# Kernel optimization log

Hardware: AMD Instinct MI355X
Metric: run time of the kernel (lower is better)

The kernel has to match this reference:

```python
import jax, jax.numpy as jnp
import numpy as np

B, NW, WL, CH, D, H, L, FF = 8, 1024, 8, 4, 512, 8, 4, 2048
K = 512  # num_masked = int(0.5 * NW)
SCALE = (D // H) ** -0.5


def _ln(x, g, b):
    m = jnp.mean(x, -1, keepdims=True)
    v = jnp.var(x, -1, keepdims=True)
    return (x - m) * jax.lax.rsqrt(v + 1e-5) * g + b


def setup_inputs():
    key = jax.random.key(0)
    ks = jax.random.split(key, 16)
    n = lambda i, shape, s=0.02: jax.random.normal(ks[i], shape, jnp.float32) * s
    return {
        "seq": jax.random.normal(ks[0], (B, NW * WL, CH), jnp.float32),
        "mask_idx": jax.lax.top_k(jax.random.uniform(ks[1], (B, NW)), K)[1].astype(jnp.int32),
        "pos_embedding": n(2, (1, NW + 1, D)),
        "mask_token": jax.random.normal(ks[3], (D,), jnp.float32),
        "pln1_g": jnp.ones((WL * CH,)), "pln1_b": jnp.zeros((WL * CH,)),
        "W_emb": n(4, (WL * CH, D)), "b_emb": jnp.zeros((D,)),
        "pln2_g": jnp.ones((D,)), "pln2_b": jnp.zeros((D,)),
        "aln_g": jnp.ones((L, D)), "aln_b": jnp.zeros((L, D)),
        "Wqkv": n(5, (L, D, 3 * D)),
        "Wo": n(6, (L, D, D)),
        "fln_g": jnp.ones((L, D)), "fln_b": jnp.zeros((L, D)),
        "Wff1": n(7, (L, D, FF)), "bff1": jnp.zeros((L, FF)),
        "Wff2": n(8, (L, FF, D)), "bff2": jnp.zeros((L, D)),
        "oln_g": jnp.ones((D,)), "oln_b": jnp.zeros((D,)),
        "W_words": n(9, (D, WL * CH)), "b_words": jnp.zeros((WL * CH,)),
    }


def reference(seq, mask_idx, pos_embedding, mask_token, pln1_g, pln1_b, W_emb, b_emb,
              pln2_g, pln2_b, aln_g, aln_b, Wqkv, Wo, fln_g, fln_b, Wff1, bff1,
              Wff2, bff2, oln_g, oln_b, W_words, b_words):
    b = seq.shape[0]
    words = seq.reshape(b, NW, WL * CH)                       # to_patch: 'b (n w) c -> b n (w c)'
    pos = pos_embedding[:, 1:NW + 1]                          # [1, NW, D]
    tokens = _ln(_ln(words, pln1_g, pln1_b) @ W_emb + b_emb, pln2_g, pln2_b) + pos
    mask_tokens = mask_token + pos                            # [1, NW, D] broadcast over batch
    bool_mask = jnp.zeros((b, NW), bool).at[jnp.arange(b)[:, None], mask_idx].set(True)
    tokens = jnp.where(bool_mask[..., None], mask_tokens, tokens)

    def block(x, p):
        h = _ln(x, p["ag"], p["ab"])
        q, k, v = [t.reshape(b, NW, H, D // H) for t in jnp.split(h @ p["Wqkv"], 3, axis=-1)]
        attn = jax.nn.softmax(jnp.einsum("bihd,bjhd->bhij", q, k) * SCALE, axis=-1)
        o = jnp.einsum("bhij,bjhd->bihd", attn, v).reshape(b, NW, D)
        x = x + o @ p["Wo"]
        h = _ln(x, p["fg"], p["fb"])
        x = x + jax.nn.gelu(h @ p["W1"] + p["b1"]) @ p["W2"] + p["b2"]
        return x, None

    layer_params = {"ag": aln_g, "ab": aln_b, "Wqkv": Wqkv, "Wo": Wo,
                    "fg": fln_g, "fb": fln_b, "W1": Wff1, "b1": bff1,
                    "W2": Wff2, "b2": bff2}
    encoded, _ = jax.lax.scan(block, tokens, layer_params)
    encoded = _ln(encoded, oln_g, oln_b)

    idx = mask_idx[..., None]
    enc_m = jnp.take_along_axis(encoded, idx, axis=1)         # [b, K, D] gather of masked positions
    pred = jax.nn.softmax((enc_m @ W_words + b_words).reshape(b, K, WL, CH), axis=-1)
    labels = jnp.take_along_axis(words, idx, axis=1).reshape(b, K, WL, CH)
    return pred, labels
```

## Files before the change

kernel.cpp:

```cpp
#include <hip/hip_runtime.h>
#include <hip/hip_bf16.h>
#include <stdint.h>


#define NTOK 8192
#define DMODEL 512
#define NHEAD 8
#define DHEAD 64
#define NWIN 1024
#define NBATCH 8
#define KMASK 512
#define FFDIM 2048
#define NLAYER 4

typedef __bf16 bf16x8 __attribute__((ext_vector_type(8)));
typedef float f32x4 __attribute__((ext_vector_type(4)));

#define MFMA16(a, b, c) __builtin_amdgcn_mfma_f32_16x16x32_bf16(a, b, c, 0, 0, 0)

static __device__ __forceinline__ void gload_lds16(const void* g, void* l) {
    __builtin_amdgcn_global_load_lds(
        (const __attribute__((address_space(1))) uint32_t*)g,
        (__attribute__((address_space(3))) uint32_t*)l, 16, 0, 0);
}

static __device__ __forceinline__ float gelu_tanh(float v) {
    float x3 = v * v * v;
    return 0.5f * v * (1.f + tanhf(0.7978845608028654f * (v + 0.044715f * x3)));
}

__global__ void embed_kernel(const float* __restrict__ seq,
                             const float* __restrict__ pos_emb,
                             const float* __restrict__ pln1_g,
                             const float* __restrict__ pln1_b,
                             const float* __restrict__ W_emb,
                             const float* __restrict__ b_emb,
                             const float* __restrict__ pln2_g,
                             const float* __restrict__ pln2_b,
                             float* __restrict__ x) {
    int tok = blockIdx.x;
    int w = tok & (NWIN - 1);
    int t = threadIdx.x;

    __shared__ float wraw[32];
    __shared__ float ln1[32];
    __shared__ float red[256], red2[256];

    if (t < 32) wraw[t] = seq[(size_t)tok * 32 + t];
    __syncthreads();

    float m = 0.f;
    for (int j = 0; j < 32; j++) m += wraw[j];
    m *= (1.f / 32.f);
    float v = 0.f;
    for (int j = 0; j < 32; j++) { float d = wraw[j] - m; v += d * d; }
    v *= (1.f / 32.f);
    float rs = rsqrtf(v + 1e-5f);
    if (t < 32) ln1[t] = (wraw[t] - m) * rs * pln1_g[t] + pln1_b[t];
    __syncthreads();

    int c0 = t, c1 = t + 256;
    float e0 = b_emb[c0];
    float e1 = b_emb[c1];
    for (int j = 0; j < 32; j++) {
        float a = ln1[j];
        e0 += a * W_emb[j * DMODEL + c0];
        e1 += a * W_emb[j * DMODEL + c1];
    }

    red[t] = e0 + e1;
    red2[t] = e0 * e0 + e1 * e1;
    __syncthreads();
    for (int o = 128; o > 0; o >>= 1) {
        if (t < o) { red[t] += red[t + o]; red2[t] += red2[t + o]; }
        __syncthreads();
    }
    float mean = red[0] * (1.f / 512.f);
    float var = red2[0] * (1.f / 512.f) - mean * mean;
    float rs2 = rsqrtf(var + 1e-5f);

    const float* pr = pos_emb + (size_t)(1 + w) * DMODEL;
    x[(size_t)tok * DMODEL + c0] =
        (e0 - mean) * rs2 * pln2_g[c0] + pln2_b[c0] + pr[c0];
    x[(size_t)tok * DMODEL + c1] =
        (e1 - mean) * rs2 * pln2_g[c1] + pln2_b[c1] + pr[c1];
}

__global__ void mask_scatter_kernel(const int* __restrict__ mask_idx,
                                    const float* __restrict__ mask_token,
                                    const float* __restrict__ pos_emb,
                                    float* __restrict__ x) {
    int bk = blockIdx.x;
    int b = bk >> 9;
    int k = bk & 511;
    int idx = mask_idx[b * KMASK + k];
    int t = threadIdx.x;
    float* row = x + (size_t)(b * NWIN + idx) * DMODEL;
    const float* pr = pos_emb + (size_t)(1 + idx) * DMODEL;
    row[t]       = mask_token[t]       + pr[t];
    row[t + 256] = mask_token[t + 256] + pr[t + 256];
}

__global__ void ln_kernel(const float* __restrict__ in,
                          __hip_bfloat16* __restrict__ out,
                          const float* __restrict__ g,
                          const float* __restrict__ bb) {
    int row = blockIdx.x;
    int t = threadIdx.x;
    const float* r = in + (size_t)row * DMODEL;
    float v0 = r[t], v1 = r[t + 256];
    float s = v0 + v1, s2 = v0 * v0 + v1 * v1;
    for (int off = 1; off < 64; off <<= 1) {
        s  += __shfl_xor(s, off);
        s2 += __shfl_xor(s2, off);
    }
    __shared__ float ws[8];
    int wave = t >> 6, lane = t & 63;
    if (lane == 0) { ws[wave] = s; ws[4 + wave] = s2; }
    __syncthreads();
    float S  = ws[0] + ws[1] + ws[2] + ws[3];
    float S2 = ws[4] + ws[5] + ws[6] + ws[7];
    float mean = S * (1.f / 512.f);
    float var = S2 * (1.f / 512.f) - mean * mean;
    float rs = rsqrtf(var + 1e-5f);
    out[(size_t)row * DMODEL + t] =
        __float2bfloat16((v0 - mean) * rs * g[t] + bb[t]);
    out[(size_t)row * DMODEL + t + 256] =
        __float2bfloat16((v1 - mean) * rs * g[t + 256] + bb[t + 256]);
}

__global__ void wconv_kernel(const float* __restrict__ src,
                             __hip_bfloat16* __restrict__ dst,
                             int K, int N) {
    int l = blockIdx.z;
    src += (size_t)l * K * N;
    dst += (size_t)l * K * N;
    __shared__ float t[32][33];
    int n0 = blockIdx.x * 32, k0 = blockIdx.y * 32;
    int tx = threadIdx.x & 31, ty = threadIdx.x >> 5;
    for (int p = 0; p < 4; p++) {
        int k = k0 + ty + p * 8;
        t[ty + p * 8][tx] = src[(size_t)k * N + n0 + tx];
    }
    __syncthreads();
    for (int p = 0; p < 4; p++) {
        int n = n0 + ty + p * 8;
        dst[(size_t)n * K + k0 + tx] = __float2bfloat16(t[tx][ty + p * 8]);
    }
}

static __device__ __forceinline__ void epi_store128(
        const float* Cs, int c, int m0, int n0, int N, int tid,
        const float* bias, const float* resid,
        float* Cf, __hip_bfloat16* Cb, int act) {
    int rl = tid >> 3;
    int cb = (tid & 7) * 16;
    int grow = m0 + c * 32 + rl;
    size_t base = (size_t)grow * N + n0 + cb;
    if (Cf) {
        for (int q = 0; q < 4; q++) {
            float4 v = *(const float4*)&Cs[rl * 132 + cb + q * 4];
            float vv[4] = {v.x, v.y, v.z, v.w};
            float4 ov;
            float* op = (float*)&ov;
            for (int e = 0; e < 4; e++) {
                float u = vv[e];
                if (bias) u += bias[n0 + cb + q * 4 + e];
                if (act == 1) u = gelu_tanh(u);
                if (resid) u += resid[base + q * 4 + e];
                op[e] = u;
            }
            *(float4*)&Cf[base + q * 4] = ov;
        }
    } else {
        for (int half = 0; half < 2; half++) {
            union { uint4 u; __hip_bfloat16 h[8]; } pk;
            for (int e = 0; e < 8; e++) {
                float u = Cs[rl * 132 + cb + half * 8 + e];
                if (bias) u += bias[n0 + cb + half * 8 + e];
                if (act == 1) u = gelu_tanh(u);
                pk.h[e] = __float2bfloat16(u);
            }
            *(uint4*)&Cb[base + half * 8] = pk.u;
        }
    }
}

static __device__ __forceinline__ void epi_store64(
        const float* Cs, int c, int m0, int n0, int N, int tid,
        const float* bias, const float* resid,
        float* Cf, __hip_bfloat16* Cb, int act) {
    int rl = tid >> 3;
    int cb = (tid & 7) * 8;
    int grow = m0 + c * 32 + rl;
    size_t base = (size_t)grow * N + n0 + cb;
    if (Cf) {
        for (int q = 0; q < 2; q++) {
            float4 v = *(const float4*)&Cs[rl * 68 + cb + q * 4];
            float vv[4] = {v.x, v.y, v.z, v.w};
            float4 ov;
            float* op = (float*)&ov;
            for (int e = 0; e < 4; e++) {
                float u = vv[e];
                if (bias) u += bias[n0 + cb + q * 4 + e];
                if (act == 1) u = gelu_tanh(u);
                if (resid) u += resid[base + q * 4 + e];
                op[e] = u;
            }
            *(float4*)&Cf[base + q * 4] = ov;
        }
    } else {
        union { uint4 u; __hip_bfloat16 h[8]; } pk;
        for (int e = 0; e < 8; e++) {
            float u = Cs[rl * 68 + cb + e];
            if (bias) u += bias[n0 + cb + e];
            if (act == 1) u = gelu_tanh(u);
            pk.h[e] = __float2bfloat16(u);
        }
        *(uint4*)&Cb[base] = pk.u;
    }
}

#define PUT128(ACC, II, JJ)                                             \
    do {                                                                \
        int rb_ = (II) * 16 + quad * 4;                                 \
        int cc_ = wc * 64 + (JJ) * 16 + l16;                            \
        Cs[(rb_ + 0) * 132 + cc_] = (ACC)[0];                           \
        Cs[(rb_ + 1) * 132 + cc_] = (ACC)[1];                           \
        Cs[(rb_ + 2) * 132 + cc_] = (ACC)[2];                           \
        Cs[(rb_ + 3) * 132 + cc_] = (ACC)[3];                           \
    } while (0)

#define CHUNK128(C, A00, A01, A02, A03, A10, A11, A12, A13)             \
    do {                                                                \
        __syncthreads();                                                \
        if (wr == ((C) >> 1)) {                                         \
            PUT128(A00, 0, 0); PUT128(A01, 0, 1);                       \
            PUT128(A02, 0, 2); PUT128(A03, 0, 3);                       \
            PUT128(A10, 1, 0); PUT128(A11, 1, 1);                       \
            PUT128(A12, 1, 2); PUT128(A13, 1, 3);                       \
        }                                                               \
        __syncthreads();                                                \
        epi_store128(Cs, (C), m0, n0, N, tid, bias, resid, Cf, Cb, act);\
    } while (0)

#define STAGE128(K0, BUF)                                               \
    do {                                                                \
        char* as_ = smem + (BUF) * 16384;                               \
        char* bs_ = as_ + 8192;                                         \
        _Pragma("unroll")                                               \
        for (int p_ = 0; p_ < 2; p_++) {                                \
            gload_lds16(Abase + (size_t)(p_ * 16) * (K * 2) + (K0) * 2, \
                        as_ + (wave * 2 + p_) * 1024);                  \
            gload_lds16(Bbase + (size_t)(p_ * 16) * (K * 2) + (K0) * 2, \
                        bs_ + (wave * 2 + p_) * 1024);                  \
        }                                                               \
    } while (0)

__global__ __launch_bounds__(256) void mfma_gemm_kernel(
        const __hip_bfloat16* __restrict__ A,
        const __hip_bfloat16* __restrict__ Bt,
        const float* __restrict__ bias,
        const float* __restrict__ resid,
        float* __restrict__ Cf,
        __hip_bfloat16* __restrict__ Cb,
        int N, int K, int act, int ntile) {
    __shared__ __align__(16) char smem[32768];
    float* Cs = (float*)smem;

    int tid = threadIdx.x;
    int wave = tid >> 6, lane = tid & 63;
    int quad = lane >> 4, l16 = lane & 15;
    int wr = wave >> 1, wc = wave & 1;

    int id = blockIdx.x;
    int slot = id >> 3;
    int mt = (id & 7) * 8 + slot / ntile;
    int nt = slot - (slot / ntile) * ntile;
    int m0 = mt * 128, n0 = nt * 128;

    f32x4 zero = {0.f, 0.f, 0.f, 0.f};
    f32x4 acc00 = zero, acc01 = zero, acc02 = zero, acc03 = zero;
    f32x4 acc10 = zero, acc11 = zero, acc12 = zero, acc13 = zero;
    f32x4 acc20 = zero, acc21 = zero, acc22 = zero, acc23 = zero;
    f32x4 acc30 = zero, acc31 = zero, acc32 = zero, acc33 = zero;

    int srow = lane >> 2;
    int schk = ((lane & 3) + (lane >> 4)) & 3;
    const char* Abase = (const char*)A +
        ((size_t)(m0 + wave * 32 + srow) * K + schk * 8) * 2;
    const char* Bbase = (const char*)Bt +
        ((size_t)(n0 + wave * 32 + srow) * K + schk * 8) * 2;
    int soff = l16 * 4 + ((quad - (l16 >> 2)) & 3);

    int nit = K >> 5;
    STAGE128(0, 0);
    for (int it = 0; it < nit; it++) {
        __syncthreads();
        if (it + 1 < nit) STAGE128((it + 1) << 5, (it + 1) & 1);

        const __hip_bfloat16* as =
            (const __hip_bfloat16*)(smem + (it & 1) * 16384);
        const __hip_bfloat16* bs = as + 4096;

        bf16x8 a0 = *(const bf16x8*)&as[(wr * 4 + 0) * 512 + soff * 8];
        bf16x8 a1 = *(const bf16x8*)&as[(wr * 4 + 1) * 512 + soff * 8];
        bf16x8 a2 = *(const bf16x8*)&as[(wr * 4 + 2) * 512 + soff * 8];
        bf16x8 a3 = *(const bf16x8*)&as[(wr * 4 + 3) * 512 + soff * 8];
        bf16x8 b0 = *(const bf16x8*)&bs[(wc * 4 + 0) * 512 + soff * 8];
        bf16x8 b1 = *(const bf16x8*)&bs[(wc * 4 + 1) * 512 + soff * 8];
        bf16x8 b2 = *(const bf16x8*)&bs[(wc * 4 + 2) * 512 + soff * 8];
        bf16x8 b3 = *(const bf16x8*)&bs[(wc * 4 + 3) * 512 + soff * 8];

        acc00 = MFMA16(a0, b0, acc00); acc01 = MFMA16(a0, b1, acc01);
        acc02 = MFMA16(a0, b2, acc02); acc03 = MFMA16(a0, b3, acc03);
        acc10 = MFMA16(a1, b0, acc10); acc11 = MFMA16(a1, b1, acc11);
        acc12 = MFMA16(a1, b2, acc12); acc13 = MFMA16(a1, b3, acc13);
        acc20 = MFMA16(a2, b0, acc20); acc21 = MFMA16(a2, b1, acc21);
        acc22 = MFMA16(a2, b2, acc22); acc23 = MFMA16(a2, b3, acc23);
        acc30 = MFMA16(a3, b0, acc30); acc31 = MFMA16(a3, b1, acc31);
        acc32 = MFMA16(a3, b2, acc32); acc33 = MFMA16(a3, b3, acc33);
    }

    CHUNK128(0, acc00, acc01, acc02, acc03, acc10, acc11, acc12, acc13);
    CHUNK128(1, acc20, acc21, acc22, acc23, acc30, acc31, acc32, acc33);
    CHUNK128(2, acc00, acc01, acc02, acc03, acc10, acc11, acc12, acc13);
    CHUNK128(3, acc20, acc21, acc22, acc23, acc30, acc31, acc32, acc33);
}

#define PUT64v2(ACC, JJ)                                                \
    do {                                                                \
        int rb_ = (wave & 1) * 16 + quad * 4;                           \
        int cc_ = (JJ) * 16 + l16;                                      \
        Cs[(rb_ + 0) * 68 + cc_] = (ACC)[0];                            \
        Cs[(rb_ + 1) * 68 + cc_] = (ACC)[1];                            \
        Cs[(rb_ + 2) * 68 + cc_] = (ACC)[2];                            \
        Cs[(rb_ + 3) * 68 + cc_] = (ACC)[3];                            \
    } while (0)

#define CHUNK64v2(C)                                                    \
    do {                                                                \
        __syncthreads();                                                \
        if ((wave >> 1) == (C)) {                                       \
            PUT64v2(acc0, 0); PUT64v2(acc1, 1);                         \
            PUT64v2(acc2, 2); PUT64v2(acc3, 3);                         \
        }                                                               \
        __syncthreads();                                                \
        epi_store64(Cs, (C), m0, n0, N, tid, bias, resid, Cf, Cb, act); \
    } while (0)

#define STAGE64v2(K0, BUF)                                              \
    do {                                                                \
        char* as_ = smem + (BUF) * 8192;                                \
        char* bs_ = as_ + 4096;                                         \
        gload_lds16(Abase + (K0) * 2, as_ + wave * 1024);               \
        gload_lds16(Bbase + (K0) * 2, bs_ + wave * 1024);               \
    } while (0)

__global__ __launch_bounds__(256) void mfma_gemm_64_kernel(
        const __hip_bfloat16* __restrict__ A,
        const __hip_bfloat16* __restrict__ Bt,
        const float* __restrict__ bias,
        const float* __restrict__ resid,
        float* __restrict__ Cf,
        __hip_bfloat16* __restrict__ Cb,
        int N, int K, int act, int ntile) {
    __shared__ __align__(16) char smem[16384];
    float* Cs = (float*)smem;

    int tid = threadIdx.x;
    int wave = tid >> 6, lane = tid & 63;
    int quad = lane >> 4, l16 = lane & 15;

    int id = blockIdx.x;
    int slot = id >> 3;
    int mt = (id & 7) * 16 + slot / ntile;
    int nt = slot - (slot / ntile) * ntile;
    int m0 = mt * 64, n0 = nt * 64;

    f32x4 zero = {0.f, 0.f, 0.f, 0.f};
    f32x4 acc0 = zero, acc1 = zero, acc2 = zero, acc3 = zero;

    int srow = lane >> 2;
    int schk = ((lane & 3) + (lane >> 4)) & 3;
    const char* Abase = (const char*)A +
        ((size_t)(m0 + wave * 16 + srow) * K + schk * 8) * 2;
    const char* Bbase = (const char*)Bt +
        ((size_t)(n0 + wave * 16 + srow) * K + schk * 8) * 2;
    int soff = l16 * 4 + ((quad - (l16 >> 2)) & 3);

    int nit = K >> 5;
    STAGE64v2(0, 0);
    for (int it = 0; it < nit; it++) {
        __syncthreads();
        if (it + 1 < nit) STAGE64v2((it + 1) << 5, (it + 1) & 1);

        const __hip_bfloat16* as =
            (const __hip_bfloat16*)(smem + (it & 1) * 8192);
        const __hip_bfloat16* bs = as + 2048;

        bf16x8 a0 = *(const bf16x8*)&as[wave * 512 + soff * 8];
        bf16x8 b0 = *(const bf16x8*)&bs[0 * 512 + soff * 8];
        bf16x8 b1 = *(const bf16x8*)&bs[1 * 512 + soff * 8];
        bf16x8 b2 = *(const bf16x8*)&bs[2 * 512 + soff * 8];
        bf16x8 b3 = *(const bf16x8*)&bs[3 * 512 + soff * 8];

        acc0 = MFMA16(a0, b0, acc0); acc1 = MFMA16(a0, b1, acc1);
        acc2 = MFMA16(a0, b2, acc2); acc3 = MFMA16(a0, b3, acc3);
    }

    CHUNK64v2(0);
    CHUNK64v2(1);
}

#define KP 72
__global__ __launch_bounds__(256) void attn_mfma_kernel(
        const __hip_bfloat16* __restrict__ qkv,
        __hip_bfloat16* __restrict__ o) {
    int id = blockIdx.x;
    int slot = id >> 3;
    int bh = (id & 7) * 8 + (slot >> 3);
    int itile = slot & 7;
    int b = bh >> 3, hh = bh & 7;

    int tid = threadIdx.x;
    int wave = tid >> 6, lane = tid & 63;
    int quad = lane >> 4, l16 = lane & 15;
    int i0 = itile * 128;

    __shared__ __align__(16) __hip_bfloat16 Ks[64 * KP];
    __shared__ __align__(16) __hip_bfloat16 Vt[64 * KP];
    __shared__ __align__(16) __hip_bfloat16 Ps[4][16 * KP];

    bf16x8 aq[2][2];
#pragma unroll
    for (int g = 0; g < 2; g++) {
        const __hip_bfloat16* qrow =
            qkv + (size_t)(b * NWIN + i0 + g * 64 + wave * 16 + l16) * 1536 + hh * 64;
        aq[g][0] = *(const bf16x8*)(qrow + quad * 8);
        aq[g][1] = *(const bf16x8*)(qrow + 32 + quad * 8);
    }

    float lp[2][4];
    f32x4 acc[2][4];
    f32x4 zero = {0.f, 0.f, 0.f, 0.f};
#pragma unroll
    for (int g = 0; g < 2; g++)
#pragma unroll
        for (int n = 0; n < 4; n++) { acc[g][n] = zero; lp[g][n] = 0.f; }

    for (int kt = 0; kt < 16; kt++) {
        int k0 = kt * 64;
        __syncthreads();

#pragma unroll
        for (int p = 0; p < 2; p++) {
            int f = p * 256 + tid;
            int r = f >> 3;
            int j = f & 7;
            int c8 = j * 8;
            const __hip_bfloat16* kp =
                qkv + (size_t)(b * NWIN + k0 + r) * 1536 + 512 + hh * 64 + c8;
            *(uint4*)&Ks[r * KP + c8] = *(const uint4*)kp;
            union { uint4 u; __hip_bfloat16 h[8]; } vv;
            vv.u = *(const uint4*)(qkv + (size_t)(b * NWIN + k0 + r) * 1536 +
                                   1024 + hh * 64 + c8);
            int colb = (((r >> 3) ^ j) << 3) + (r & 7);
#pragma unroll
            for (int u = 0; u < 8; u++) Vt[(c8 + u) * KP + colb] = vv.h[u];
        }
        __syncthreads();

        bf16x8 bk[4][2], bv[4][2];
#pragma unroll
        for (int n = 0; n < 4; n++) {
            int key = n * 16 + l16;
            bk[n][0] = *(const bf16x8*)&Ks[key * KP + quad * 8];
            bk[n][1] = *(const bf16x8*)&Ks[key * KP + 32 + quad * 8];
            int d = n * 16 + l16;
            int sw = (d >> 3) & 7;
            bv[n][0] = *(const bf16x8*)&Vt[d * KP + ((quad ^ sw) << 3)];
            bv[n][1] = *(const bf16x8*)&Vt[d * KP + (((quad + 4) ^ sw) << 3)];
        }

#pragma unroll
        for (int g = 0; g < 2; g++) {
            f32x4 s[4];
#pragma unroll
            for (int n = 0; n < 4; n++) {
                f32x4 t = zero;
                t = MFMA16(aq[g][0], bk[n][0], t);
                t = MFMA16(aq[g][1], bk[n][1], t);
                s[n] = t;
            }
#pragma unroll
            for (int r = 0; r < 4; r++) {
                float ls = 0.f;
#pragma unroll
                for (int n = 0; n < 4; n++) {
                    float pv = __expf(s[n][r] * 0.125f);
                    Ps[wave][(quad * 4 + r) * KP + n * 16 + l16] =
                        __float2bfloat16(pv);
                    ls += pv;
                }
                lp[g][r] += ls;
            }
            bf16x8 ap0 = *(const bf16x8*)&Ps[wave][l16 * KP + quad * 8];
            bf16x8 ap1 = *(const bf16x8*)&Ps[wave][l16 * KP + 32 + quad * 8];
#pragma unroll
            for (int n = 0; n < 4; n++) {
                acc[g][n] = MFMA16(ap0, bv[n][0], acc[g][n]);
                acc[g][n] = MFMA16(ap1, bv[n][1], acc[g][n]);
            }
        }
    }

#pragma unroll
    for (int g = 0; g < 2; g++) {
#pragma unroll
        for (int r = 0; r < 4; r++) {
            float ls = lp[g][r];
            ls += __shfl_xor(ls, 1);
            ls += __shfl_xor(ls, 2);
            ls += __shfl_xor(ls, 4);
            ls += __shfl_xor(ls, 8);
            float invl = 1.f / ls;
            int row = i0 + g * 64 + wave * 16 + quad * 4 + r;
#pragma unroll
            for (int n = 0; n < 4; n++) {
                o[(size_t)(b * NWIN + row) * DMODEL + hh * 64 + n * 16 + l16] =
                    __float2bfloat16(acc[g][n][r] * invl);
            }
        }
    }
}

__global__ void out_kernel(const float* __restrict__ x,
                           const int* __restrict__ mask_idx,
                           const float* __restrict__ oln_g,
                           const float* __restrict__ oln_b,
                           const float* __restrict__ W_words,
                           const float* __restrict__ b_words,
                           const float* __restrict__ seq,
                           float* __restrict__ out) {
    int k = blockIdx.x, b = blockIdx.y;
    int idx = mask_idx[b * KMASK + k];
    int t = threadIdx.x;
    const float* row = x + (size_t)(b * NWIN + idx) * DMODEL;
    float v0 = row[t], v1 = row[t + 256];

    __shared__ float red[256], red2[256];
    __shared__ float sh[512];
    __shared__ float part[256];
    __shared__ float lg[32];

    red[t] = v0 + v1;
    red2[t] = v0 * v0 + v1 * v1;
    __syncthreads();
    for (int o = 128; o > 0; o >>= 1) {
        if (t < o) { red[t] += red[t + o]; red2[t] += red2[t + o]; }
        __syncthreads();
    }
    float mean = red[0] * (1.f / 512.f);
    float var = red2[0] * (1.f / 512.f) - mean * mean;
    float rs = rsqrtf(var + 1e-5f);
    sh[t]       = (v0 - mean) * rs * oln_g[t] + oln_b[t];
    sh[t + 256] = (v1 - mean) * rs * oln_g[t + 256] + oln_b[t + 256];
    __syncthreads();

    int c = t & 31, ch = t >> 5;
    float p = 0.f;
    for (int j = ch * 64; j < ch * 64 + 64; j++)
        p += sh[j] * W_words[j * 32 + c];
    part[t] = p;
    __syncthreads();
    if (t < 32) {
        float s = b_words[t];
        for (int u = 0; u < 8; u++) s += part[u * 32 + t];
        lg[t] = s;
    }
    __syncthreads();

    size_t obase = (size_t)(b * KMASK + k) * 32;
    if (t < 32) {
        int g0 = t & ~3;
        float mx = fmaxf(fmaxf(lg[g0], lg[g0 + 1]), fmaxf(lg[g0 + 2], lg[g0 + 3]));
        float s = expf(lg[g0] - mx) + expf(lg[g0 + 1] - mx) +
                  expf(lg[g0 + 2] - mx) + expf(lg[g0 + 3] - mx);
        out[obase + t] = expf(lg[t] - mx) / s;
        out[131072 + obase + t] = seq[(size_t)b * 32768 + (size_t)idx * 32 + t];
    }
}

extern "C" void kernel_launch(void* const* d_in, const int* in_sizes, int n_in,
                              void* d_out, int out_size, void* d_ws, size_t ws_size,
                              hipStream_t stream) {
    const float* seq      = (const float*)d_in[0];
    const int*   mask_idx = (const int*)d_in[1];
    const float* pos_emb  = (const float*)d_in[2];
    const float* mask_tok = (const float*)d_in[3];
    const float* pln1_g   = (const float*)d_in[4];
    const float* pln1_b   = (const float*)d_in[5];
    const float* W_emb    = (const float*)d_in[6];
    const float* b_emb    = (const float*)d_in[7];
    const float* pln2_g   = (const float*)d_in[8];
    const float* pln2_b   = (const float*)d_in[9];
    const float* aln_g    = (const float*)d_in[10];
    const float* aln_b    = (const float*)d_in[11];
    const float* Wqkv     = (const float*)d_in[12];
    const float* Wo       = (const float*)d_in[13];
    const float* fln_g    = (const float*)d_in[14];
    const float* fln_b    = (const float*)d_in[15];
    const float* Wff1     = (const float*)d_in[16];
    const float* bff1     = (const float*)d_in[17];
    const float* Wff2     = (const float*)d_in[18];
    const float* bff2     = (const float*)d_in[19];
    const float* oln_g    = (const float*)d_in[20];
    const float* oln_b    = (const float*)d_in[21];
    const float* W_words  = (const float*)d_in[22];
    const float* b_words  = (const float*)d_in[23];

    uint8_t* ws = (uint8_t*)d_ws;
    float* x = (float*)ws;
    __hip_bfloat16* qkv_bf = (__hip_bfloat16*)(ws + 16777216);
    __hip_bfloat16* ff_bf  = qkv_bf;
    __hip_bfloat16* h_bf   = (__hip_bfloat16*)(ws + 50331648);
    __hip_bfloat16* o_bf   = (__hip_bfloat16*)(ws + 58720256);
    __hip_bfloat16* wqkv_t = (__hip_bfloat16*)(ws + 67108864);
    __hip_bfloat16* wo_t   = wqkv_t + (size_t)NLAYER * DMODEL * 3 * DMODEL;
    __hip_bfloat16* wff1_t = wo_t   + (size_t)NLAYER * DMODEL * DMODEL;
    __hip_bfloat16* wff2_t = wff1_t + (size_t)NLAYER * DMODEL * FFDIM;

    wconv_kernel<<<dim3(48, 16, NLAYER), 256, 0, stream>>>(Wqkv, wqkv_t, DMODEL, 3 * DMODEL);
    wconv_kernel<<<dim3(16, 16, NLAYER), 256, 0, stream>>>(Wo,   wo_t,   DMODEL, DMODEL);
    wconv_kernel<<<dim3(64, 16, NLAYER), 256, 0, stream>>>(Wff1, wff1_t, DMODEL, FFDIM);
    wconv_kernel<<<dim3(16, 64, NLAYER), 256, 0, stream>>>(Wff2, wff2_t, FFDIM, DMODEL);

    embed_kernel<<<NTOK, 256, 0, stream>>>(seq, pos_emb, pln1_g, pln1_b,
                                           W_emb, b_emb, pln2_g, pln2_b, x);
    mask_scatter_kernel<<<NBATCH * KMASK, 256, 0, stream>>>(mask_idx, mask_tok, pos_emb, x);

    for (int l = 0; l < NLAYER; l++) {
        ln_kernel<<<NTOK, 256, 0, stream>>>(x, h_bf, aln_g + l * DMODEL, aln_b + l * DMODEL);
        mfma_gemm_kernel<<<64 * 12, 256, 0, stream>>>(
            h_bf, wqkv_t + (size_t)l * DMODEL * 3 * DMODEL,
            nullptr, nullptr, nullptr, qkv_bf, 3 * DMODEL, DMODEL, 0, 12);
        attn_mfma_kernel<<<512, 256, 0, stream>>>(qkv_bf, o_bf);
        mfma_gemm_64_kernel<<<128 * 8, 256, 0, stream>>>(
            o_bf, wo_t + (size_t)l * DMODEL * DMODEL,
            nullptr, x, x, nullptr, DMODEL, DMODEL, 0, 8);
        ln_kernel<<<NTOK, 256, 0, stream>>>(x, h_bf, fln_g + l * DMODEL, fln_b + l * DMODEL);
        mfma_gemm_kernel<<<64 * 16, 256, 0, stream>>>(
            h_bf, wff1_t + (size_t)l * DMODEL * FFDIM,
            bff1 + (size_t)l * FFDIM, nullptr, nullptr, ff_bf, FFDIM, DMODEL, 1, 16);
        mfma_gemm_64_kernel<<<128 * 8, 256, 0, stream>>>(
            ff_bf, wff2_t + (size_t)l * FFDIM * DMODEL,
            bff2 + (size_t)l * DMODEL, x, x, nullptr, DMODEL, FFDIM, 0, 8);
    }

    out_kernel<<<dim3(KMASK, NBATCH), 256, 0, stream>>>(
        x, mask_idx, oln_g, oln_b, W_words, b_words, seq, (float*)d_out);
}
```

Measured before the change: 882.2 us.

## Split attention over two key halves with a combine kernel; use a sigmoid-form GELU

The attention kernel now splits the key range into two halves, so the grid doubles from 512 to 1024 blocks. Each block writes unnormalized partial outputs and row sums. A new combine kernel adds the two partials and divides by the summed denominators. Separately, the tanh GELU is rewritten in its equivalent sigmoid form using __expf. The aim is better CU occupancy for attention and cheaper GELU math, at the cost of an extra kernel launch and extra partial-buffer traffic that reuses workspace regions.

```diff
diff --git a/kernel.cpp b/kernel.cpp
--- a/kernel.cpp
+++ b/kernel.cpp
@@ -25,8 +25,8 @@
 }
 
 static __device__ __forceinline__ float gelu_tanh(float v) {
-    float x3 = v * v * v;
-    return 0.5f * v * (1.f + tanhf(0.7978845608028654f * (v + 0.044715f * x3)));
+    float u = 1.5957691216f * (v + 0.044715f * v * v * v);
+    return v / (1.f + __expf(-u));
 }
 
 __global__ void embed_kernel(const float* __restrict__ seq,
@@ -416,11 +416,13 @@
 #define KP 72
 __global__ __launch_bounds__(256) void attn_mfma_kernel(
         const __hip_bfloat16* __restrict__ qkv,
-        __hip_bfloat16* __restrict__ o) {
+        __hip_bfloat16* __restrict__ opart,
+        float* __restrict__ lpart) {
     int id = blockIdx.x;
     int slot = id >> 3;
-    int bh = (id & 7) * 8 + (slot >> 3);
-    int itile = slot & 7;
+    int bh = (id & 7) * 8 + (slot >> 4);
+    int itile = (slot >> 1) & 7;
+    int split = slot & 1;
     int b = bh >> 3, hh = bh & 7;
 
     int tid = threadIdx.x;
@@ -449,7 +451,7 @@
 #pragma unroll
         for (int n = 0; n < 4; n++) { acc[g][n] = zero; lp[g][n] = 0.f; }
 
-    for (int kt = 0; kt < 16; kt++) {
+    for (int kt = split * 8; kt < split * 8 + 8; kt++) {
         int k0 = kt * 64;
         __syncthreads();
 
@@ -524,14 +526,32 @@
             ls += __shfl_xor(ls, 2);
             ls += __shfl_xor(ls, 4);
             ls += __shfl_xor(ls, 8);
-            float invl = 1.f / ls;
             int row = i0 + g * 64 + wave * 16 + quad * 4 + r;
+            size_t tok = (size_t)(b * NWIN + row);
+            if (l16 == 0)
+                lpart[(size_t)split * NTOK * NHEAD + tok * NHEAD + hh] = ls;
 #pragma unroll
             for (int n = 0; n < 4; n++) {
-                o[(size_t)(b * NWIN + row) * DMODEL + hh * 64 + n * 16 + l16] =
-                    __float2bfloat16(acc[g][n][r] * invl);
+                opart[(size_t)split * NTOK * DMODEL + tok * DMODEL +
+                      hh * 64 + n * 16 + l16] = __float2bfloat16(acc[g][n][r]);
             }
         }
+    }
+}
+
+__global__ void attn_combine_kernel(const __hip_bfloat16* __restrict__ opart,
+                                    const float* __restrict__ lpart,
+                                    __hip_bfloat16* __restrict__ o) {
+    size_t tok = blockIdx.x;
+    int t = threadIdx.x;
+    for (int half = 0; half < 2; half++) {
+        int d = t + half * 256;
+        int hh = d >> 6;
+        float l0 = lpart[tok * NHEAD + hh];
+        float l1 = lpart[(size_t)NTOK * NHEAD + tok * NHEAD + hh];
+        float o0 = __bfloat162float(opart[tok * DMODEL + d]);
+        float o1 = __bfloat162float(opart[(size_t)NTOK * DMODEL + tok * DMODEL + d]);
+        o[tok * DMODEL + d] = __float2bfloat16((o0 + o1) / (l0 + l1));
     }
 }
 
@@ -624,6 +644,8 @@
     float* x = (float*)ws;
     __hip_bfloat16* qkv_bf = (__hip_bfloat16*)(ws + 16777216);
     __hip_bfloat16* ff_bf  = qkv_bf;
+    float* lpart           = (float*)(ws + 46137344);
+    __hip_bfloat16* opart  = (__hip_bfloat16*)(ws + 50331648);
     __hip_bfloat16* h_bf   = (__hip_bfloat16*)(ws + 50331648);
     __hip_bfloat16* o_bf   = (__hip_bfloat16*)(ws + 58720256);
     __hip_bfloat16* wqkv_t = (__hip_bfloat16*)(ws + 67108864);
@@ -645,7 +667,8 @@
         mfma_gemm_kernel<<<64 * 12, 256, 0, stream>>>(
             h_bf, wqkv_t + (size_t)l * DMODEL * 3 * DMODEL,
             nullptr, nullptr, nullptr, qkv_bf, 3 * DMODEL, DMODEL, 0, 12);
-        attn_mfma_kernel<<<512, 256, 0, stream>>>(qkv_bf, o_bf);
+        attn_mfma_kernel<<<1024, 256, 0, stream>>>(qkv_bf, opart, lpart);
+        attn_combine_kernel<<<NTOK, 256, 0, stream>>>(opart, lpart, o_bf);
         mfma_gemm_64_kernel<<<128 * 8, 256, 0, stream>>>(
             o_bf, wo_t + (size_t)l * DMODEL * DMODEL,
             nullptr, x, x, nullptr, DMODEL, DMODEL, 0, 8);
```

Result: no change. 898.8 us (+1.9%).
